# Kernel tuning notes

Measured on AMD Instinct MI355X. Metric: run time of the kernel, lower is better.

The kernel has to match this reference:

```python
import jax, jax.numpy as jnp
import numpy as np

N_PAPER, N_AUTHOR, N_INST = 500000, 300000, 10000
D = 128
E_CITES = E_WRITES = E_REV = 2000000
E_AFF = 500000


def _sage(x_src, x_dst, src, dst, Wl, bl, Wr):
    """PyG SAGEConv (mean aggr): lin_l(mean_{j->i} x_j) + lin_r(x_i).
    lin_l has bias, lin_r does not. Isolated dst nodes get zero mean."""
    n_dst = x_dst.shape[0]
    msg_sum = jax.ops.segment_sum(x_src[src], dst, num_segments=n_dst)  # [n_dst, D]
    cnt = jax.ops.segment_sum(jnp.ones(src.shape, x_src.dtype), dst, num_segments=n_dst)
    mean = msg_sum / jnp.maximum(cnt, 1.0)[:, None]
    return mean @ Wl + bl + x_dst @ Wr


def setup_inputs() -> dict:
    key = jax.random.key(0)
    ks = jax.random.split(key, 24)
    s = 1.0 / np.sqrt(D)
    inp = {
        'x_paper': jax.random.normal(ks[0], (N_PAPER, D), jnp.float32),
        'x_author': jax.random.normal(ks[1], (N_AUTHOR, D), jnp.float32),
        'x_inst': jax.random.normal(ks[2], (N_INST, D), jnp.float32),
        'cites_src': jax.random.randint(ks[3], (E_CITES,), 0, N_PAPER, jnp.int32),
        'cites_dst': jax.random.randint(ks[4], (E_CITES,), 0, N_PAPER, jnp.int32),
        'writes_src': jax.random.randint(ks[5], (E_WRITES,), 0, N_AUTHOR, jnp.int32),
        'writes_dst': jax.random.randint(ks[6], (E_WRITES,), 0, N_PAPER, jnp.int32),
        'rev_src': jax.random.randint(ks[7], (E_REV,), 0, N_PAPER, jnp.int32),
        'rev_dst': jax.random.randint(ks[8], (E_REV,), 0, N_AUTHOR, jnp.int32),
        'aff_src': jax.random.randint(ks[9], (E_AFF,), 0, N_AUTHOR, jnp.int32),
        'aff_dst': jax.random.randint(ks[10], (E_AFF,), 0, N_INST, jnp.int32),
    }
    names = ['cites', 'writes', 'rev', 'aff']
    for i, name in enumerate(names):
        kw = jax.random.split(ks[11 + i], 3)
        inp[f'Wl_{name}'] = jax.random.normal(kw[0], (D, D), jnp.float32) * s
        inp[f'bl_{name}'] = jnp.zeros((D,), jnp.float32)
        inp[f'Wr_{name}'] = jax.random.normal(kw[1], (D, D), jnp.float32) * s
    return inp


def reference(x_paper, x_author, x_inst,
              cites_src, cites_dst, writes_src, writes_dst,
              rev_src, rev_dst, aff_src, aff_dst,
              Wl_cites, bl_cites, Wr_cites,
              Wl_writes, bl_writes, Wr_writes,
              Wl_rev, bl_rev, Wr_rev,
              Wl_aff, bl_aff, Wr_aff):
    # HeteroConv sums per-relation SAGEConv outputs sharing a dst node type,
    # then the layer applies activation (relu) per node type. Dropout=0 (eval).
    h_paper = jax.nn.relu(
        _sage(x_paper, x_paper, cites_src, cites_dst, Wl_cites, bl_cites, Wr_cites)
        + _sage(x_author, x_paper, writes_src, writes_dst, Wl_writes, bl_writes, Wr_writes))
    h_author = jax.nn.relu(
        _sage(x_paper, x_author, rev_src, rev_dst, Wl_rev, bl_rev, Wr_rev))
    h_inst = jax.nn.relu(
        _sage(x_author, x_inst, aff_src, aff_dst, Wl_aff, bl_aff, Wr_aff))
    return h_paper, h_author, h_inst
```

## Files before the change

### kernel.cpp

```cpp
#include <hip/hip_runtime.h>

#define N_PAPER  500000
#define N_AUTHOR 300000
#define N_INST   10000
#define E_CITES  2000000
#define E_WRITES 2000000
#define E_REV    2000000
#define E_AFF    500000
#define E_TOT    (E_CITES + E_WRITES + E_REV + E_AFF)

#define SLOT_CITES  0
#define SLOT_WRITES (N_PAPER)
#define SLOT_REV    (2 * N_PAPER)
#define SLOT_AFF    (2 * N_PAPER + N_AUTHOR)
#define NSLOT       (2 * N_PAPER + N_AUTHOR + N_INST)

__device__ __forceinline__ float4 f4zero() { return make_float4(0.f, 0.f, 0.f, 0.f); }
__device__ __forceinline__ float4 f4add(float4 a, float4 b) {
    return make_float4(a.x + b.x, a.y + b.y, a.z + b.z, a.w + b.w);
}
__device__ __forceinline__ float4 f4scale(float4 a, float s) {
    return make_float4(a.x * s, a.y * s, a.z * s, a.w * s);
}
__device__ __forceinline__ float4 f4fma(float4 acc, float s, float4 w) {
    acc.x = fmaf(s, w.x, acc.x);
    acc.y = fmaf(s, w.y, acc.y);
    acc.z = fmaf(s, w.z, acc.z);
    acc.w = fmaf(s, w.w, acc.w);
    return acc;
}
__device__ __forceinline__ float4 f4relu(float4 a) {
    return make_float4(fmaxf(a.x, 0.f), fmaxf(a.y, 0.f), fmaxf(a.z, 0.f), fmaxf(a.w, 0.f));
}

__global__ void count_edges(const int* __restrict__ cd, const int* __restrict__ wd,
                            const int* __restrict__ rd, const int* __restrict__ ad,
                            int* __restrict__ cnt) {
    int t = blockIdx.x * 256 + threadIdx.x;
    if (t >= E_TOT) return;
    int slot;
    if (t < E_CITES)                          slot = SLOT_CITES  + cd[t];
    else if (t < E_CITES + E_WRITES)          slot = SLOT_WRITES + wd[t - E_CITES];
    else if (t < E_CITES + E_WRITES + E_REV)  slot = SLOT_REV    + rd[t - (E_CITES + E_WRITES)];
    else                                      slot = SLOT_AFF    + ad[t - (E_CITES + E_WRITES + E_REV)];
    atomicAdd(&cnt[slot], 1);
}

__global__ void alloc_csr(const int* __restrict__ cnt, int* __restrict__ start,
                          int* __restrict__ cursor, int* __restrict__ pool) {
    int i = blockIdx.x * 256 + threadIdx.x;
    int deg = (i < NSLOT) ? cnt[i] : 0;
    int incl = deg;
    #pragma unroll
    for (int d = 1; d < 64; d <<= 1) {
        int v = __shfl_up(incl, d);
        if ((threadIdx.x & 63) >= d) incl += v;
    }
    int total = __shfl(incl, 63);
    int base = 0;
    if ((threadIdx.x & 63) == 63) base = atomicAdd(pool, total);
    base = __shfl(base, 63);
    if (i < NSLOT) {
        int s = base + incl - deg;
        start[i]  = s;
        cursor[i] = s;
    }
}

__global__ void fill_csr(const int* __restrict__ cs, const int* __restrict__ cd,
                         const int* __restrict__ wsrc, const int* __restrict__ wd,
                         const int* __restrict__ rs, const int* __restrict__ rd,
                         const int* __restrict__ asrc, const int* __restrict__ ad,
                         int* __restrict__ cursor, int* __restrict__ esrc) {
    int t = blockIdx.x * 256 + threadIdx.x;
    if (t >= E_TOT) return;
    int src, slot;
    if (t < E_CITES)                         { src = cs[t];                              slot = SLOT_CITES  + cd[t]; }
    else if (t < E_CITES + E_WRITES)         { int u = t - E_CITES;                      src = wsrc[u]; slot = SLOT_WRITES + wd[u]; }
    else if (t < E_CITES + E_WRITES + E_REV) { int u = t - (E_CITES + E_WRITES);         src = rs[u];   slot = SLOT_REV    + rd[u]; }
    else                                     { int u = t - (E_CITES + E_WRITES + E_REV); src = asrc[u]; slot = SLOT_AFF    + ad[u]; }
    int pos = atomicAdd(&cursor[slot], 1);
    esrc[pos] = src;
}

__global__ void wprep(const float* __restrict__ Wl_c, const float* __restrict__ bl_c, const float* __restrict__ Wr_c,
                      const float* __restrict__ Wl_w, const float* __restrict__ bl_w, const float* __restrict__ Wr_w,
                      const float* __restrict__ Wl_r, const float* __restrict__ bl_r, const float* __restrict__ Wr_r,
                      const float* __restrict__ Wl_a, const float* __restrict__ bl_a, const float* __restrict__ Wr_a,
                      float* __restrict__ Wp, float* __restrict__ Wa, float* __restrict__ Wi,
                      float* __restrict__ bp, float* __restrict__ ba, float* __restrict__ bi) {
    int t = blockIdx.x * 256 + threadIdx.x;
    if (t < 384 * 128) {
        int k = t >> 7, j = t & 127;
        float v;
        if (k < 128)      v = Wl_c[t];
        else if (k < 256) v = Wl_w[(k - 128) * 128 + j];
        else              v = Wr_c[(k - 256) * 128 + j] + Wr_w[(k - 256) * 128 + j];
        Wp[t] = v;
    }
    if (t < 256 * 128) {
        int k = t >> 7, j = t & 127;
        Wa[t] = (k < 128) ? Wl_r[t] : Wr_r[(k - 128) * 128 + j];
        Wi[t] = (k < 128) ? Wl_a[t] : Wr_a[(k - 128) * 128 + j];
    }
    if (t < 128) {
        bp[t] = bl_c[t] + bl_w[t];
        ba[t] = bl_r[t];
        bi[t] = bl_a[t];
    }
}

template <int NREL>
__global__ __launch_bounds__(256) void sage_fused(
        const float* __restrict__ xdst,
        const float* __restrict__ xs0, const float* __restrict__ xs1,
        int slotbase0, int slotbase1,
        const int* __restrict__ cnt, const int* __restrict__ start,
        const int* __restrict__ esrc,
        const float* __restrict__ W, const float* __restrict__ bias,
        float* __restrict__ out, int nrows) {
    const int K   = (NREL + 1) * 128;
    const int LDT = K + 4;
    __shared__ float tile[32 * ((NREL + 1) * 128 + 4)];

    const int tid = threadIdx.x;
    {
        const int r   = tid >> 3;
        const int sub = tid & 7;
        const int c0  = sub * 16;
        const int row = blockIdx.x * 32 + r;
        float* trow = &tile[r * LDT];
        if (row < nrows) {
            {
                int slot = slotbase0 + row;
                int c = cnt[slot], s = start[slot];
                float4 a0 = f4zero(), a1 = f4zero(), a2 = f4zero(), a3 = f4zero();
                for (int e = 0; e < c; ++e) {
                    int j = esrc[s + e];
                    const float4* p = (const float4*)(xs0 + (size_t)j * 128 + c0);
                    a0 = f4add(a0, p[0]); a1 = f4add(a1, p[1]);
                    a2 = f4add(a2, p[2]); a3 = f4add(a3, p[3]);
                }
                float sc = 1.0f / (float)max(c, 1);
                float4* d = (float4*)(trow + c0);
                d[0] = f4scale(a0, sc); d[1] = f4scale(a1, sc);
                d[2] = f4scale(a2, sc); d[3] = f4scale(a3, sc);
            }
            if (NREL == 2) {
                int slot = slotbase1 + row;
                int c = cnt[slot], s = start[slot];
                float4 a0 = f4zero(), a1 = f4zero(), a2 = f4zero(), a3 = f4zero();
                for (int e = 0; e < c; ++e) {
                    int j = esrc[s + e];
                    const float4* p = (const float4*)(xs1 + (size_t)j * 128 + c0);
                    a0 = f4add(a0, p[0]); a1 = f4add(a1, p[1]);
                    a2 = f4add(a2, p[2]); a3 = f4add(a3, p[3]);
                }
                float sc = 1.0f / (float)max(c, 1);
                float4* d = (float4*)(trow + 128 + c0);
                d[0] = f4scale(a0, sc); d[1] = f4scale(a1, sc);
                d[2] = f4scale(a2, sc); d[3] = f4scale(a3, sc);
            }
            {
                const float4* p = (const float4*)(xdst + (size_t)row * 128 + c0);
                float4* d = (float4*)(trow + NREL * 128 + c0);
                d[0] = p[0]; d[1] = p[1]; d[2] = p[2]; d[3] = p[3];
            }
        } else {
            float4* d0 = (float4*)(trow + c0);
            float4 z = f4zero();
            d0[0] = z; d0[1] = z; d0[2] = z; d0[3] = z;
            if (NREL == 2) {
                float4* d1 = (float4*)(trow + 128 + c0);
                d1[0] = z; d1[1] = z; d1[2] = z; d1[3] = z;
            }
            float4* d2 = (float4*)(trow + NREL * 128 + c0);
            d2[0] = z; d2[1] = z; d2[2] = z; d2[3] = z;
        }
    }
    __syncthreads();

    {
        const int rg = tid >> 5;
        const int cg = tid & 31;
        float4 acc0 = f4zero(), acc1 = f4zero(), acc2 = f4zero(), acc3 = f4zero();
        const float* tA = &tile[(rg * 4) * LDT];
        #pragma unroll 4
        for (int k = 0; k < K; k += 4) {
            const float* wbase = W + (size_t)k * 128 + cg * 4;
            float4 w0 = *(const float4*)(wbase);
            float4 w1 = *(const float4*)(wbase + 128);
            float4 w2 = *(const float4*)(wbase + 256);
            float4 w3 = *(const float4*)(wbase + 384);
            float4 aA = *(const float4*)(tA + k);
            float4 aB = *(const float4*)(tA + LDT + k);
            float4 aC = *(const float4*)(tA + 2 * LDT + k);
            float4 aD = *(const float4*)(tA + 3 * LDT + k);
            acc0 = f4fma(acc0, aA.x, w0); acc0 = f4fma(acc0, aA.y, w1);
            acc0 = f4fma(acc0, aA.z, w2); acc0 = f4fma(acc0, aA.w, w3);
            acc1 = f4fma(acc1, aB.x, w0); acc1 = f4fma(acc1, aB.y, w1);
            acc1 = f4fma(acc1, aB.z, w2); acc1 = f4fma(acc1, aB.w, w3);
            acc2 = f4fma(acc2, aC.x, w0); acc2 = f4fma(acc2, aC.y, w1);
            acc2 = f4fma(acc2, aC.z, w2); acc2 = f4fma(acc2, aC.w, w3);
            acc3 = f4fma(acc3, aD.x, w0); acc3 = f4fma(acc3, aD.y, w1);
            acc3 = f4fma(acc3, aD.z, w2); acc3 = f4fma(acc3, aD.w, w3);
        }
        float4 b = *(const float4*)(bias + cg * 4);
        int row0 = blockIdx.x * 32 + rg * 4;
        if (row0 + 0 < nrows) *(float4*)(out + (size_t)(row0 + 0) * 128 + cg * 4) = f4relu(f4add(acc0, b));
        if (row0 + 1 < nrows) *(float4*)(out + (size_t)(row0 + 1) * 128 + cg * 4) = f4relu(f4add(acc1, b));
        if (row0 + 2 < nrows) *(float4*)(out + (size_t)(row0 + 2) * 128 + cg * 4) = f4relu(f4add(acc2, b));
        if (row0 + 3 < nrows) *(float4*)(out + (size_t)(row0 + 3) * 128 + cg * 4) = f4relu(f4add(acc3, b));
    }
}

extern "C" void kernel_launch(void* const* d_in, const int* in_sizes, int n_in,
                              void* d_out, int out_size, void* d_ws, size_t ws_size,
                              hipStream_t stream) {
    const float* x_paper  = (const float*)d_in[0];
    const float* x_author = (const float*)d_in[1];
    const float* x_inst   = (const float*)d_in[2];
    const int* cites_src  = (const int*)d_in[3];
    const int* cites_dst  = (const int*)d_in[4];
    const int* writes_src = (const int*)d_in[5];
    const int* writes_dst = (const int*)d_in[6];
    const int* rev_src    = (const int*)d_in[7];
    const int* rev_dst    = (const int*)d_in[8];
    const int* aff_src    = (const int*)d_in[9];
    const int* aff_dst    = (const int*)d_in[10];
    const float* Wl_c = (const float*)d_in[11];
    const float* bl_c = (const float*)d_in[12];
    const float* Wr_c = (const float*)d_in[13];
    const float* Wl_w = (const float*)d_in[14];
    const float* bl_w = (const float*)d_in[15];
    const float* Wr_w = (const float*)d_in[16];
    const float* Wl_r = (const float*)d_in[17];
    const float* bl_r = (const float*)d_in[18];
    const float* Wr_r = (const float*)d_in[19];
    const float* Wl_a = (const float*)d_in[20];
    const float* bl_a = (const float*)d_in[21];
    const float* Wr_a = (const float*)d_in[22];

    float* out = (float*)d_out;

    char* ws = (char*)d_ws;
    size_t off = 0;
    int* cnt    = (int*)(ws + off); off += (size_t)NSLOT * 4;
    int* pool   = (int*)(ws + off); off += 32;
    int* start  = (int*)(ws + off); off += (size_t)NSLOT * 4;
    int* cursor = (int*)(ws + off); off += (size_t)NSLOT * 4;
    int* esrc   = (int*)(ws + off); off += (size_t)E_TOT * 4;
    float* Wp   = (float*)(ws + off); off += 384 * 128 * 4;
    float* Wa   = (float*)(ws + off); off += 256 * 128 * 4;
    float* Wi   = (float*)(ws + off); off += 256 * 128 * 4;
    float* bp   = (float*)(ws + off); off += 512;
    float* ba   = (float*)(ws + off); off += 512;
    float* bi   = (float*)(ws + off); off += 512;
    (void)ws_size; (void)out_size; (void)n_in; (void)in_sizes;

    hipMemsetAsync(ws, 0, (size_t)NSLOT * 4 + 32, stream);

    const int eblocks = (E_TOT + 255) / 256;
    count_edges<<<eblocks, 256, 0, stream>>>(cites_dst, writes_dst, rev_dst, aff_dst, cnt);
    alloc_csr<<<(NSLOT + 255) / 256, 256, 0, stream>>>(cnt, start, cursor, pool);
    fill_csr<<<eblocks, 256, 0, stream>>>(cites_src, cites_dst, writes_src, writes_dst,
                                          rev_src, rev_dst, aff_src, aff_dst, cursor, esrc);
    wprep<<<(384 * 128 + 255) / 256, 256, 0, stream>>>(
        Wl_c, bl_c, Wr_c, Wl_w, bl_w, Wr_w, Wl_r, bl_r, Wr_r, Wl_a, bl_a, Wr_a,
        Wp, Wa, Wi, bp, ba, bi);

    sage_fused<2><<<(N_PAPER + 31) / 32, 256, 0, stream>>>(
        x_paper, x_paper, x_author, SLOT_CITES, SLOT_WRITES,
        cnt, start, esrc, Wp, bp, out, N_PAPER);
    sage_fused<1><<<(N_AUTHOR + 31) / 32, 256, 0, stream>>>(
        x_author, x_paper, nullptr, SLOT_REV, 0,
        cnt, start, esrc, Wa, ba, out + (size_t)N_PAPER * 128, N_AUTHOR);
    sage_fused<1><<<(N_INST + 31) / 32, 256, 0, stream>>>(
        x_inst, x_author, nullptr, SLOT_AFF, 0,
        cnt, start, esrc, Wi, bi, out + (size_t)(N_PAPER + N_AUTHOR) * 128, N_INST);
}
```

Before: 3.342 ms.

## Use split-bf16 MFMA for SAGE linear layers with swizzled LDS tiles

```diff
diff --git a/kernel.cpp b/kernel.cpp
--- a/kernel.cpp
+++ b/kernel.cpp
@@ -15,22 +15,16 @@
 #define SLOT_AFF    (2 * N_PAPER + N_AUTHOR)
 #define NSLOT       (2 * N_PAPER + N_AUTHOR + N_INST)
 
-__device__ __forceinline__ float4 f4zero() { return make_float4(0.f, 0.f, 0.f, 0.f); }
-__device__ __forceinline__ float4 f4add(float4 a, float4 b) {
-    return make_float4(a.x + b.x, a.y + b.y, a.z + b.z, a.w + b.w);
-}
-__device__ __forceinline__ float4 f4scale(float4 a, float s) {
-    return make_float4(a.x * s, a.y * s, a.z * s, a.w * s);
-}
-__device__ __forceinline__ float4 f4fma(float4 acc, float s, float4 w) {
-    acc.x = fmaf(s, w.x, acc.x);
-    acc.y = fmaf(s, w.y, acc.y);
-    acc.z = fmaf(s, w.z, acc.z);
-    acc.w = fmaf(s, w.w, acc.w);
-    return acc;
-}
-__device__ __forceinline__ float4 f4relu(float4 a) {
-    return make_float4(fmaxf(a.x, 0.f), fmaxf(a.y, 0.f), fmaxf(a.z, 0.f), fmaxf(a.w, 0.f));
+typedef short  bf16x8 __attribute__((ext_vector_type(8)));
+typedef float  f32x4  __attribute__((ext_vector_type(4)));
+
+__device__ __forceinline__ unsigned short f2b(float f) {
+    unsigned int u = __float_as_uint(f);
+    unsigned int r = (u + 0x7FFFu + ((u >> 16) & 1u)) >> 16;
+    return (unsigned short)r;
+}
+__device__ __forceinline__ float b2f(unsigned short h) {
+    return __uint_as_float(((unsigned int)h) << 16);
 }
 
 __global__ void count_edges(const int* __restrict__ cd, const int* __restrict__ wd,
@@ -83,11 +77,17 @@
     esrc[pos] = src;
 }
 
+__device__ __forceinline__ int frag_idx(int k, int col) {
+    return (((k >> 5) * 4 + ((k >> 3) & 3)) * 128 + col) * 8 + (k & 7);
+}
+
 __global__ void wprep(const float* __restrict__ Wl_c, const float* __restrict__ bl_c, const float* __restrict__ Wr_c,
                       const float* __restrict__ Wl_w, const float* __restrict__ bl_w, const float* __restrict__ Wr_w,
                       const float* __restrict__ Wl_r, const float* __restrict__ bl_r, const float* __restrict__ Wr_r,
                       const float* __restrict__ Wl_a, const float* __restrict__ bl_a, const float* __restrict__ Wr_a,
-                      float* __restrict__ Wp, float* __restrict__ Wa, float* __restrict__ Wi,
+                      unsigned short* __restrict__ Wp_hi, unsigned short* __restrict__ Wp_lo,
+                      unsigned short* __restrict__ Wa_hi, unsigned short* __restrict__ Wa_lo,
+                      unsigned short* __restrict__ Wi_hi, unsigned short* __restrict__ Wi_lo,
                       float* __restrict__ bp, float* __restrict__ ba, float* __restrict__ bi) {
     int t = blockIdx.x * 256 + threadIdx.x;
     if (t < 384 * 128) {
@@ -96,12 +96,18 @@
         if (k < 128)      v = Wl_c[t];
         else if (k < 256) v = Wl_w[(k - 128) * 128 + j];
         else              v = Wr_c[(k - 256) * 128 + j] + Wr_w[(k - 256) * 128 + j];
-        Wp[t] = v;
+        unsigned short hi = f2b(v);
+        unsigned short lo = f2b(v - b2f(hi));
+        int idx = frag_idx(k, j);
+        Wp_hi[idx] = hi; Wp_lo[idx] = lo;
     }
     if (t < 256 * 128) {
         int k = t >> 7, j = t & 127;
-        Wa[t] = (k < 128) ? Wl_r[t] : Wr_r[(k - 128) * 128 + j];
-        Wi[t] = (k < 128) ? Wl_a[t] : Wr_a[(k - 128) * 128 + j];
+        float va = (k < 128) ? Wl_r[t] : Wr_r[(k - 128) * 128 + j];
+        float vi = (k < 128) ? Wl_a[t] : Wr_a[(k - 128) * 128 + j];
+        int idx = frag_idx(k, j);
+        unsigned short ha = f2b(va); Wa_hi[idx] = ha; Wa_lo[idx] = f2b(va - b2f(ha));
+        unsigned short hx = f2b(vi); Wi_hi[idx] = hx; Wi_lo[idx] = f2b(vi - b2f(hx));
     }
     if (t < 128) {
         bp[t] = bl_c[t] + bl_w[t];
@@ -111,106 +117,140 @@
 }
 
 template <int NREL>
-__global__ __launch_bounds__(256) void sage_fused(
+__global__ __launch_bounds__(256) void sage_mfma(
         const float* __restrict__ xdst,
         const float* __restrict__ xs0, const float* __restrict__ xs1,
         int slotbase0, int slotbase1,
         const int* __restrict__ cnt, const int* __restrict__ start,
         const int* __restrict__ esrc,
-        const float* __restrict__ W, const float* __restrict__ bias,
+        const unsigned short* __restrict__ Wf_hi, const unsigned short* __restrict__ Wf_lo,
+        const float* __restrict__ bias,
         float* __restrict__ out, int nrows) {
-    const int K   = (NREL + 1) * 128;
-    const int LDT = K + 4;
-    __shared__ float tile[32 * ((NREL + 1) * 128 + 4)];
-
-    const int tid = threadIdx.x;
-    {
-        const int r   = tid >> 3;
-        const int sub = tid & 7;
-        const int c0  = sub * 16;
-        const int row = blockIdx.x * 32 + r;
-        float* trow = &tile[r * LDT];
+    constexpr int K  = (NREL + 1) * 128;
+    constexpr int K2 = K * 2;
+    constexpr int KB = K / 32;
+    __shared__ unsigned short lds_hi[32 * K];
+    __shared__ unsigned short lds_lo[32 * K];
+    char* chi = (char*)lds_hi;
+    char* clo = (char*)lds_lo;
+
+    const int tid  = threadIdx.x;
+    const int w    = tid >> 6;
+    const int lane = tid & 63;
+
+    for (int i = 0; i < 8; ++i) {
+        const int tr   = w * 8 + i;
+        const int row  = blockIdx.x * 32 + tr;
+        const int swz  = (tr & 7) << 4;
+        const int kbyte = lane * 4;
         if (row < nrows) {
-            {
-                int slot = slotbase0 + row;
-                int c = cnt[slot], s = start[slot];
-                float4 a0 = f4zero(), a1 = f4zero(), a2 = f4zero(), a3 = f4zero();
-                for (int e = 0; e < c; ++e) {
+            #pragma unroll
+            for (int rel = 0; rel < NREL; ++rel) {
+                const float* xs = (rel == 0) ? xs0 : xs1;
+                const int slot  = (rel == 0 ? slotbase0 : slotbase1) + row;
+                const int c = cnt[slot], s = start[slot];
+                float a0 = 0.f, a1 = 0.f;
+                int e = 0;
+                for (; e + 4 <= c; e += 4) {
+                    int j0 = esrc[s + e], j1 = esrc[s + e + 1];
+                    int j2 = esrc[s + e + 2], j3 = esrc[s + e + 3];
+                    float2 v0 = *(const float2*)(xs + (size_t)j0 * 128 + lane * 2);
+                    float2 v1 = *(const float2*)(xs + (size_t)j1 * 128 + lane * 2);
+                    float2 v2 = *(const float2*)(xs + (size_t)j2 * 128 + lane * 2);
+                    float2 v3 = *(const float2*)(xs + (size_t)j3 * 128 + lane * 2);
+                    a0 += (v0.x + v1.x) + (v2.x + v3.x);
+                    a1 += (v0.y + v1.y) + (v2.y + v3.y);
+                }
+                for (; e < c; ++e) {
                     int j = esrc[s + e];
-                    const float4* p = (const float4*)(xs0 + (size_t)j * 128 + c0);
-                    a0 = f4add(a0, p[0]); a1 = f4add(a1, p[1]);
-                    a2 = f4add(a2, p[2]); a3 = f4add(a3, p[3]);
+                    float2 v = *(const float2*)(xs + (size_t)j * 128 + lane * 2);
+                    a0 += v.x; a1 += v.y;
                 }
-                float sc = 1.0f / (float)max(c, 1);
-                float4* d = (float4*)(trow + c0);
-                d[0] = f4scale(a0, sc); d[1] = f4scale(a1, sc);
-                d[2] = f4scale(a2, sc); d[3] = f4scale(a3, sc);
-            }
-            if (NREL == 2) {
-                int slot = slotbase1 + row;
-                int c = cnt[slot], s = start[slot];
-                float4 a0 = f4zero(), a1 = f4zero(), a2 = f4zero(), a3 = f4zero();
-                for (int e = 0; e < c; ++e) {
-                    int j = esrc[s + e];
-                    const float4* p = (const float4*)(xs1 + (size_t)j * 128 + c0);
-                    a0 = f4add(a0, p[0]); a1 = f4add(a1, p[1]);
-                    a2 = f4add(a2, p[2]); a3 = f4add(a3, p[3]);
-                }
-                float sc = 1.0f / (float)max(c, 1);
-                float4* d = (float4*)(trow + 128 + c0);
-                d[0] = f4scale(a0, sc); d[1] = f4scale(a1, sc);
-                d[2] = f4scale(a2, sc); d[3] = f4scale(a3, sc);
+                const float sc = 1.0f / (float)(c > 0 ? c : 1);
+                a0 *= sc; a1 *= sc;
+                unsigned short h0 = f2b(a0), h1 = f2b(a1);
+                float l0 = a0 - b2f(h0), l1 = a1 - b2f(h1);
+                int off = (tr * K2 + rel * 256 + kbyte) ^ swz;
+                *(unsigned int*)(chi + off) = (unsigned int)h0 | ((unsigned int)h1 << 16);
+                *(unsigned int*)(clo + off) = (unsigned int)f2b(l0) | ((unsigned int)f2b(l1) << 16);
             }
             {
-                const float4* p = (const float4*)(xdst + (size_t)row * 128 + c0);
-                float4* d = (float4*)(trow + NREL * 128 + c0);
-                d[0] = p[0]; d[1] = p[1]; d[2] = p[2]; d[3] = p[3];
+                float2 v = *(const float2*)(xdst + (size_t)row * 128 + lane * 2);
+                unsigned short h0 = f2b(v.x), h1 = f2b(v.y);
+                float l0 = v.x - b2f(h0), l1 = v.y - b2f(h1);
+                int off = (tr * K2 + NREL * 256 + kbyte) ^ swz;
+                *(unsigned int*)(chi + off) = (unsigned int)h0 | ((unsigned int)h1 << 16);
+                *(unsigned int*)(clo + off) = (unsigned int)f2b(l0) | ((unsigned int)f2b(l1) << 16);
             }
         } else {
-            float4* d0 = (float4*)(trow + c0);
-            float4 z = f4zero();
-            d0[0] = z; d0[1] = z; d0[2] = z; d0[3] = z;
-            if (NREL == 2) {
-                float4* d1 = (float4*)(trow + 128 + c0);
-                d1[0] = z; d1[1] = z; d1[2] = z; d1[3] = z;
+            #pragma unroll
+            for (int rel = 0; rel <= NREL; ++rel) {
+                int off = (tr * K2 + rel * 256 + kbyte) ^ swz;
+                *(unsigned int*)(chi + off) = 0u;
+                *(unsigned int*)(clo + off) = 0u;
             }
-            float4* d2 = (float4*)(trow + NREL * 128 + c0);
-            d2[0] = z; d2[1] = z; d2[2] = z; d2[3] = z;
         }
     }
     __syncthreads();
 
-    {
-        const int rg = tid >> 5;
-        const int cg = tid & 31;
-        float4 acc0 = f4zero(), acc1 = f4zero(), acc2 = f4zero(), acc3 = f4zero();
-        const float* tA = &tile[(rg * 4) * LDT];
-        #pragma unroll 4
-        for (int k = 0; k < K; k += 4) {
-            const float* wbase = W + (size_t)k * 128 + cg * 4;
-            float4 w0 = *(const float4*)(wbase);
-            float4 w1 = *(const float4*)(wbase + 128);
-            float4 w2 = *(const float4*)(wbase + 256);
-            float4 w3 = *(const float4*)(wbase + 384);
-            float4 aA = *(const float4*)(tA + k);
-            float4 aB = *(const float4*)(tA + LDT + k);
-            float4 aC = *(const float4*)(tA + 2 * LDT + k);
-            float4 aD = *(const float4*)(tA + 3 * LDT + k);
-            acc0 = f4fma(acc0, aA.x, w0); acc0 = f4fma(acc0, aA.y, w1);
-            acc0 = f4fma(acc0, aA.z, w2); acc0 = f4fma(acc0, aA.w, w3);
-            acc1 = f4fma(acc1, aB.x, w0); acc1 = f4fma(acc1, aB.y, w1);
-            acc1 = f4fma(acc1, aB.z, w2); acc1 = f4fma(acc1, aB.w, w3);
-            acc2 = f4fma(acc2, aC.x, w0); acc2 = f4fma(acc2, aC.y, w1);
-            acc2 = f4fma(acc2, aC.z, w2); acc2 = f4fma(acc2, aC.w, w3);
-            acc3 = f4fma(acc3, aD.x, w0); acc3 = f4fma(acc3, aD.y, w1);
-            acc3 = f4fma(acc3, aD.z, w2); acc3 = f4fma(acc3, aD.w, w3);
+    const int l15 = lane & 15;
+    const int lg  = lane >> 4;
+    const int colbase = w * 32 + l15;
+    const int aswz = (l15 & 7) << 4;
+
+    f32x4 acc00 = {0.f, 0.f, 0.f, 0.f};
+    f32x4 acc01 = {0.f, 0.f, 0.f, 0.f};
+    f32x4 acc10 = {0.f, 0.f, 0.f, 0.f};
+    f32x4 acc11 = {0.f, 0.f, 0.f, 0.f};
+
+    for (int kb = 0; kb < KB; ++kb) {
+        const int ab  = kb * 64 + lg * 16;
+        const int o0  = ((l15)      * K2 + ab) ^ aswz;
+        const int o1  = ((l15 + 16) * K2 + ab) ^ aswz;
+        bf16x8 a0h = *(const bf16x8*)(chi + o0);
+        bf16x8 a1h = *(const bf16x8*)(chi + o1);
+        bf16x8 a0l = *(const bf16x8*)(clo + o0);
+        bf16x8 a1l = *(const bf16x8*)(clo + o1);
+
+        const size_t g0 = ((size_t)(kb * 4 + lg) * 128 + colbase) * 8;
+        const size_t g1 = g0 + 16 * 8;
+        bf16x8 w0h = *(const bf16x8*)(Wf_hi + g0);
+        bf16x8 w1h = *(const bf16x8*)(Wf_hi + g1);
+        bf16x8 w0l = *(const bf16x8*)(Wf_lo + g0);
+        bf16x8 w1l = *(const bf16x8*)(Wf_lo + g1);
+
+        acc00 = __builtin_amdgcn_mfma_f32_16x16x32_bf16(a0h, w0h, acc00, 0, 0, 0);
+        acc00 = __builtin_amdgcn_mfma_f32_16x16x32_bf16(a0l, w0h, acc00, 0, 0, 0);
+        acc00 = __builtin_amdgcn_mfma_f32_16x16x32_bf16(a0h, w0l, acc00, 0, 0, 0);
+
+        acc01 = __builtin_amdgcn_mfma_f32_16x16x32_bf16(a0h, w1h, acc01, 0, 0, 0);
+        acc01 = __builtin_amdgcn_mfma_f32_16x16x32_bf16(a0l, w1h, acc01, 0, 0, 0);
+        acc01 = __builtin_amdgcn_mfma_f32_16x16x32_bf16(a0h, w1l, acc01, 0, 0, 0);
+
+        acc10 = __builtin_amdgcn_mfma_f32_16x16x32_bf16(a1h, w0h, acc10, 0, 0, 0);
+        acc10 = __builtin_amdgcn_mfma_f32_16x16x32_bf16(a1l, w0h, acc10, 0, 0, 0);
+        acc10 = __builtin_amdgcn_mfma_f32_16x16x32_bf16(a1h, w0l, acc10, 0, 0, 0);
+
+        acc11 = __builtin_amdgcn_mfma_f32_16x16x32_bf16(a1h, w1h, acc11, 0, 0, 0);
+        acc11 = __builtin_amdgcn_mfma_f32_16x16x32_bf16(a1l, w1h, acc11, 0, 0, 0);
+        acc11 = __builtin_amdgcn_mfma_f32_16x16x32_bf16(a1h, w1l, acc11, 0, 0, 0);
+    }
+
+    const float b0 = bias[colbase];
+    const float b1 = bias[colbase + 16];
+    const int row0 = blockIdx.x * 32 + lg * 4;
+    #pragma unroll
+    for (int j = 0; j < 4; ++j) {
+        int r = row0 + j;
+        if (r < nrows) {
+            out[(size_t)r * 128 + colbase]      = fmaxf(acc00[j] + b0, 0.f);
+            out[(size_t)r * 128 + colbase + 16] = fmaxf(acc01[j] + b1, 0.f);
         }
-        float4 b = *(const float4*)(bias + cg * 4);
-        int row0 = blockIdx.x * 32 + rg * 4;
-        if (row0 + 0 < nrows) *(float4*)(out + (size_t)(row0 + 0) * 128 + cg * 4) = f4relu(f4add(acc0, b));
-        if (row0 + 1 < nrows) *(float4*)(out + (size_t)(row0 + 1) * 128 + cg * 4) = f4relu(f4add(acc1, b));
-        if (row0 + 2 < nrows) *(float4*)(out + (size_t)(row0 + 2) * 128 + cg * 4) = f4relu(f4add(acc2, b));
-        if (row0 + 3 < nrows) *(float4*)(out + (size_t)(row0 + 3) * 128 + cg * 4) = f4relu(f4add(acc3, b));
+        int r2 = r + 16;
+        if (r2 < nrows) {
+            out[(size_t)r2 * 128 + colbase]      = fmaxf(acc10[j] + b0, 0.f);
+            out[(size_t)r2 * 128 + colbase + 16] = fmaxf(acc11[j] + b1, 0.f);
+        }
     }
 }
 
@@ -250,9 +290,12 @@
     int* start  = (int*)(ws + off); off += (size_t)NSLOT * 4;
     int* cursor = (int*)(ws + off); off += (size_t)NSLOT * 4;
     int* esrc   = (int*)(ws + off); off += (size_t)E_TOT * 4;
-    float* Wp   = (float*)(ws + off); off += 384 * 128 * 4;
-    float* Wa   = (float*)(ws + off); off += 256 * 128 * 4;
-    float* Wi   = (float*)(ws + off); off += 256 * 128 * 4;
+    unsigned short* Wp_hi = (unsigned short*)(ws + off); off += 384 * 128 * 2;
+    unsigned short* Wp_lo = (unsigned short*)(ws + off); off += 384 * 128 * 2;
+    unsigned short* Wa_hi = (unsigned short*)(ws + off); off += 256 * 128 * 2;
+    unsigned short* Wa_lo = (unsigned short*)(ws + off); off += 256 * 128 * 2;
+    unsigned short* Wi_hi = (unsigned short*)(ws + off); off += 256 * 128 * 2;
+    unsigned short* Wi_lo = (unsigned short*)(ws + off); off += 256 * 128 * 2;
     float* bp   = (float*)(ws + off); off += 512;
     float* ba   = (float*)(ws + off); off += 512;
     float* bi   = (float*)(ws + off); off += 512;
@@ -267,15 +310,15 @@
                                           rev_src, rev_dst, aff_src, aff_dst, cursor, esrc);
     wprep<<<(384 * 128 + 255) / 256, 256, 0, stream>>>(
         Wl_c, bl_c, Wr_c, Wl_w, bl_w, Wr_w, Wl_r, bl_r, Wr_r, Wl_a, bl_a, Wr_a,
-        Wp, Wa, Wi, bp, ba, bi);
-
-    sage_fused<2><<<(N_PAPER + 31) / 32, 256, 0, stream>>>(
+        Wp_hi, Wp_lo, Wa_hi, Wa_lo, Wi_hi, Wi_lo, bp, ba, bi);
+
+    sage_mfma<2><<<(N_PAPER + 31) / 32, 256, 0, stream>>>(
         x_paper, x_paper, x_author, SLOT_CITES, SLOT_WRITES,
-        cnt, start, esrc, Wp, bp, out, N_PAPER);
-    sage_fused<1><<<(N_AUTHOR + 31) / 32, 256, 0, stream>>>(
+        cnt, start, esrc, Wp_hi, Wp_lo, bp, out, N_PAPER);
+    sage_mfma<1><<<(N_AUTHOR + 31) / 32, 256, 0, stream>>>(
         x_author, x_paper, nullptr, SLOT_REV, 0,
-        cnt, start, esrc, Wa, ba, out + (size_t)N_PAPER * 128, N_AUTHOR);
-    sage_fused<1><<<(N_INST + 31) / 32, 256, 0, stream>>>(
+        cnt, start, esrc, Wa_hi, Wa_lo, ba, out + (size_t)N_PAPER * 128, N_AUTHOR);
+    sage_mfma<1><<<(N_INST + 31) / 32, 256, 0, stream>>>(
         x_inst, x_author, nullptr, SLOT_AFF, 0,
-        cnt, start, esrc, Wi, bi, out + (size_t)(N_PAPER + N_AUTHOR) * 128, N_INST);
-}
+        cnt, start, esrc, Wi_hi, Wi_lo, bi, out + (size_t)(N_PAPER + N_AUTHOR) * 128, N_INST);
+}
```

Result: faster. 3.198 ms (-4.3%).
